# Performance work log

Measured on AMD Instinct MI355X. Metric: run time of the kernel, lower is better.

The kernel has to match this reference:

```python
import jax, jax.numpy as jnp
import numpy as np

L, H, N = 131072, 256, 128
P = N // 2  # conj-symmetric half state


def _hippo_params(p_sz, h_sz):
    # create_DPLR_HiPPO(block_size) in numpy (float64 eigh, then cast)
    n = np.arange(p_sz)
    pv = np.sqrt(1.0 + 2.0 * n)
    A = -(np.tril(np.outer(pv, pv)) - np.diag(n))          # make_HiPPO
    Pl = np.sqrt(n + 0.5)
    Bl = np.sqrt(2.0 * n + 1.0)
    S = A + np.outer(Pl, Pl)                                # normal part
    lam_re = np.full(p_sz, S.diagonal().mean())
    lam_im, V = np.linalg.eigh(S * (-1j))
    Lambda = lam_re + 1j * lam_im                           # (P,)
    Vinv = V.conj().T
    rng = np.random.default_rng(0)
    B0 = rng.normal(size=(p_sz, h_sz)) / np.sqrt(h_sz)      # lecun-normal-ish
    Bc = Vinv @ B0                                          # init_VinvB -> (P,H) complex
    C0 = rng.normal(size=(h_sz, p_sz)) / np.sqrt(p_sz)
    Cc = C0 @ V                                             # init_CV -> (H,P) complex
    Dv = rng.normal(size=(h_sz,))
    return Lambda, Bc, Cc, Dv


def setup_inputs() -> dict:
    Lambda, Bc, Cc, Dv = _hippo_params(P, H)
    deltas = np.logspace(-3.0, -1.0, P)
    key = jax.random.key(0)
    ku, kd = jax.random.split(key)
    u = jax.random.normal(ku, (L, H), dtype=jnp.float32)
    d = jax.random.bernoulli(kd, 1.0 / 1024.0, (L,))        # sparse episode resets
    f32 = lambda a: jnp.asarray(a, dtype=jnp.float32)
    return {
        "u": u,
        "Lambda_re": f32(Lambda.real), "Lambda_im": f32(Lambda.imag),
        "B_re": f32(Bc.real), "B_im": f32(Bc.imag),
        "C_re": f32(Cc.real), "C_im": f32(Cc.imag),
        "D": f32(Dv),
        "deltas": f32(deltas),
        "x0_re": jnp.zeros((P,), jnp.float32), "x0_im": jnp.zeros((P,), jnp.float32),
        "d": d,
    }


def reference(u, Lambda_re, Lambda_im, B_re, B_im, C_re, C_im, D, deltas,
              x0_re, x0_im, d):
    cplx = jnp.complex64
    Lambda = (Lambda_re + 1j * Lambda_im).astype(cplx)      # (P,)
    B = (B_re + 1j * B_im).astype(cplx)                     # (P,H)
    C = (C_re + 1j * C_im).astype(cplx)                     # (H,P)
    x0 = (x0_re + 1j * x0_im).astype(cplx)                  # (P,)

    # ZOH discretization
    Lambda_bar = jnp.exp(Lambda * deltas)                   # (P,)
    B_bar = ((Lambda_bar - 1.0) / Lambda)[:, None] * B      # (P,H)

    Bu = u.astype(cplx) @ B_bar.T                           # (L,P)

    Lseq = u.shape[0]
    A_el = jnp.concatenate([jnp.ones((1, Lambda_bar.shape[0]), cplx),
                            jnp.broadcast_to(Lambda_bar, (Lseq, Lambda_bar.shape[0]))])
    b_el = jnp.concatenate([x0[None, :], Bu])
    d_el = jnp.concatenate([jnp.zeros((1,), bool), d])

    def comb(qi, qj):
        Ai, bi, di = qi
        Aj, bj, dj = qj
        m = dj[..., None]
        A = jnp.where(m, Aj, Aj * Ai)
        b = jnp.where(m, bj, Aj * bi + bj)
        return (A, b, jnp.logical_or(di, dj))

    _, xs, _ = jax.lax.associative_scan(comb, (A_el, b_el, d_el))
    xs = xs[1:]                                             # (L,P)

    # conj-symmetric readout: y = 2*Re(C x) + D*u
    y = 2.0 * (xs @ C.T).real + u * D                       # (L,H)
    return y
```

## Files before the change

### kernel.cpp

```cpp
#include <hip/hip_runtime.h>
#include <hip/hip_bf16.h>
#include <stdint.h>

#define L_SEQ 131072
#define H_DIM 256
#define P_DIM 64
#define C2    128
#define T_CH  128
#define NC    1024
#define SUBT  32
#define BPAD  136

typedef unsigned short u16t;
typedef __attribute__((ext_vector_type(8))) short short8;
typedef __attribute__((ext_vector_type(4))) float f32x4;

#define OFF_W2_U   32768u
#define OFF_LPRE_F 32768u
#define OFF_LPIM_F 40960u
#define OFF_LAMB_F 49152u
#define OFF_FR_I   49408u
#define OFF_CL_F   50432u
#define OFF_XIN_F  181504u
#define OFF_U16_B  2097152u

__device__ __forceinline__ float bf2f(unsigned v){
    return __builtin_bit_cast(float, v << 16);
}
__device__ __forceinline__ u16t f2bf16(float f){
    uint32_t u = __builtin_bit_cast(uint32_t, f);
    u += 0x7fffu + ((u >> 16) & 1u);
    return (u16t)(u >> 16);
}
__device__ __forceinline__ unsigned pk2(float a, float b){
    return (unsigned)f2bf16(a) | ((unsigned)f2bf16(b) << 16);
}

__global__ void k0a(const float* __restrict__ Lre, const float* __restrict__ Lim,
                    const float* __restrict__ deltas, float* __restrict__ wsf){
    int p = threadIdx.x;
    if (p >= P_DIM) return;
    float lr = Lre[p], li = Lim[p], dl = deltas[p];
    float er = expf(lr * dl);
    float si, co;
    sincosf(li * dl, &si, &co);
    float lbr = er * co, lbi = er * si;
    float den = lr*lr + li*li;
    float gr = ((lbr - 1.f)*lr + lbi*li) / den;
    float gi = (lbi*lr - (lbr - 1.f)*li) / den;
    float* lamb = wsf + OFF_LAMB_F;
    lamb[p] = lbr; lamb[64+p] = lbi; lamb[128+p] = gr; lamb[192+p] = gi;
    float* lpre = wsf + OFF_LPRE_F;
    float* lpim = wsf + OFF_LPIM_F;
    float pr = lbr, pi = lbi;
    for (int k = 0; k < T_CH; k++){
        lpre[k*64 + p] = pr;
        lpim[k*64 + p] = pi;
        float nr = pr*lbr - pi*lbi;
        float ni = pr*lbi + pi*lbr;
        pr = nr; pi = ni;
    }
}

__global__ void k0b(const float* __restrict__ Bre, const float* __restrict__ Bim,
                    const float* __restrict__ Cre, const float* __restrict__ Cim,
                    float* __restrict__ wsf, u16t* __restrict__ wsu){
    int idx = blockIdx.x * 256 + threadIdx.x;
    const float* lamb = wsf + OFF_LAMB_F;
    if (idx < 32768){
        int c = idx >> 8, h = idx & 255;
        int p = c & 63;
        float gr = lamb[128+p], gi = lamb[192+p];
        float br = Bre[p*H_DIM + h], bi = Bim[p*H_DIM + h];
        float v = (c < 64) ? (gr*br - gi*bi) : (gr*bi + gi*br);
        wsu[idx] = f2bf16(v);
    } else {
        int i2 = idx - 32768;
        int h = i2 >> 7, c = i2 & 127;
        float v = (c < 64) ? 2.f * Cre[h*P_DIM + c] : -2.f * Cim[h*P_DIM + (c-64)];
        wsu[OFF_W2_U + i2] = f2bf16(v);
    }
}

template<bool WRITE_U16>
__global__ __launch_bounds__(256, 2) void k1(const float* __restrict__ u,
                                             const int* __restrict__ dflag,
                                             float* __restrict__ wsf,
                                             u16t* __restrict__ wsu,
                                             u16t* __restrict__ u16g){
    __shared__ u16t  buf[T_CH * BPAD];
    __shared__ int   d_lds[T_CH];
    __shared__ float sublast[4*128];
    __shared__ int   sfr[4];

    const int tid  = threadIdx.x;
    const int w    = tid >> 6, lane = tid & 63;
    const int m    = lane & 15, q = lane >> 4;
    const int cc   = blockIdx.x;
    const int t0   = cc * T_CH;
    const int tg   = t0 + w * SUBT;

    if (tid < T_CH) d_lds[tid] = dflag[t0 + tid];

    const u16t* W1 = wsu;
    f32x4 acc[2][8];
    #pragma unroll
    for (int a = 0; a < 2; a++)
        #pragma unroll
        for (int b = 0; b < 8; b++) acc[a][b] = (f32x4){0.f,0.f,0.f,0.f};

    #pragma unroll
    for (int kf = 0; kf < 8; kf++){
        const int k0 = kf*32 + q*8;
        short8 afr[2];
        #pragma unroll
        for (int mt = 0; mt < 2; mt++){
            const float* ap = u + (size_t)(tg + mt*16 + m)*H_DIM + k0;
            float4 f0 = *(const float4*)ap;
            float4 f1 = *(const float4*)(ap + 4);
            uint4 pk;
            pk.x = pk2(f0.x, f0.y); pk.y = pk2(f0.z, f0.w);
            pk.z = pk2(f1.x, f1.y); pk.w = pk2(f1.z, f1.w);
            if (WRITE_U16)
                *(uint4*)(u16g + (size_t)(tg + mt*16 + m)*H_DIM + k0) = pk;
            afr[mt] = __builtin_bit_cast(short8, pk);
        }
        #pragma unroll
        for (int nt = 0; nt < 8; nt++){
            short8 bfr = __builtin_bit_cast(short8, *(const uint4*)(W1 + (nt*16 + m)*H_DIM + k0));
            acc[0][nt] = __builtin_amdgcn_mfma_f32_16x16x32_bf16(afr[0], bfr, acc[0][nt], 0,0,0);
            acc[1][nt] = __builtin_amdgcn_mfma_f32_16x16x32_bf16(afr[1], bfr, acc[1][nt], 0,0,0);
        }
    }
    #pragma unroll
    for (int mt = 0; mt < 2; mt++)
        #pragma unroll
        for (int nt = 0; nt < 8; nt++){
            int c  = nt*16 + m;
            int tl = w*SUBT + mt*16 + q*4;
            #pragma unroll
            for (int r = 0; r < 4; r++)
                buf[(tl + r)*BPAD + c] = f2bf16(acc[mt][nt][r]);
        }
    __syncthreads();

    {
        const float* lamb = wsf + OFF_LAMB_F;
        float lbr = lamb[lane], lbi = lamb[64 + lane];
        float xr = 0.f, xi = 0.f;
        int frs = SUBT;
        const int base = w * SUBT;
        for (int tt = 0; tt < SUBT; tt++){
            int tl = base + tt;
            float br = bf2f(buf[tl*BPAD + lane]);
            float bi = bf2f(buf[tl*BPAD + 64 + lane]);
            if (d_lds[tl]){
                if (frs == SUBT) frs = tt;
                xr = br; xi = bi;
            } else {
                float nr = fmaf(lbr, xr, fmaf(-lbi, xi, br));
                float ni = fmaf(lbr, xi, fmaf( lbi, xr, bi));
                xr = nr; xi = ni;
            }
        }
        sublast[w*128 + lane]      = xr;
        sublast[w*128 + 64 + lane] = xi;
        if (lane == 0) sfr[w] = frs;
    }
    __syncthreads();

    if (tid < 64){
        const float* lpre = wsf + OFF_LPRE_F;
        const float* lpim = wsf + OFF_LPIM_F;
        float l32r = lpre[(SUBT-1)*64 + tid], l32i = lpim[(SUBT-1)*64 + tid];
        float xr = 0.f, xi = 0.f;
        int fr_c = T_CH;
        #pragma unroll
        for (int w2 = 0; w2 < 4; w2++){
            float sr = sublast[w2*128 + tid], si = sublast[w2*128 + 64 + tid];
            int f = sfr[w2];
            if (f < SUBT){
                xr = sr; xi = si;
                if (fr_c == T_CH) fr_c = w2*SUBT + f;
            } else {
                float nr = fmaf(l32r, xr, fmaf(-l32i, xi, sr));
                float ni = fmaf(l32r, xi, fmaf( l32i, xr, si));
                xr = nr; xi = ni;
            }
        }
        float* clast = wsf + OFF_CL_F;
        clast[cc*128 + tid]      = xr;
        clast[cc*128 + 64 + tid] = xi;
        if (tid == 0) ((int*)wsf)[OFF_FR_I + cc] = fr_c;
    }
}

__global__ void k2(const float* __restrict__ x0re, const float* __restrict__ x0im,
                   float* __restrict__ wsf){
    const int p = threadIdx.x;
    const float* clast = wsf + OFF_CL_F;
    const int*   frg   = (const int*)wsf + OFF_FR_I;
    float*       xin   = wsf + OFF_XIN_F;
    const float ltr = (wsf + OFF_LPRE_F)[127*64 + p];
    const float lti = (wsf + OFF_LPIM_F)[127*64 + p];
    float xr = x0re[p], xi = x0im[p];
    const int G = 16;
    float br[G], bi[G], br2[G], bi2[G]; int fr[G], fr2[G];

    auto ldg = [&](int cb, float* A, float* B, int* F){
        #pragma unroll
        for (int j = 0; j < G; j++){
            A[j] = clast[(cb+j)*128 + p];
            B[j] = clast[(cb+j)*128 + 64 + p];
            F[j] = frg[cb+j];
        }
    };
    ldg(0, br, bi, fr);
    for (int g = 0; g < NC / G; g++){
        int cb = g * G;
        if (g + 1 < NC / G) ldg(cb + G, br2, bi2, fr2);
        #pragma unroll
        for (int j = 0; j < G; j++){
            xin[(cb+j)*128 + p]      = xr;
            xin[(cb+j)*128 + 64 + p] = xi;
            if (fr[j] < T_CH){ xr = br[j]; xi = bi[j]; }
            else {
                float nr = fmaf(ltr, xr, fmaf(-lti, xi, br[j]));
                float ni = fmaf(ltr, xi, fmaf( lti, xr, bi[j]));
                xr = nr; xi = ni;
            }
        }
        #pragma unroll
        for (int j = 0; j < G; j++){ br[j]=br2[j]; bi[j]=bi2[j]; fr[j]=fr2[j]; }
    }
}

template<bool USE_U16>
__global__ __launch_bounds__(256, 2) void k3(const float* __restrict__ u,
                                             const u16t* __restrict__ u16g,
                                             const int* __restrict__ dflag,
                                             const float* __restrict__ D,
                                             float* __restrict__ wsf,
                                             u16t* __restrict__ wsu,
                                             float* __restrict__ y){
    __shared__ u16t  buf[T_CH * BPAD];
    __shared__ int   d_lds[T_CH];
    __shared__ float sublast[4*128];
    __shared__ float xin_s[4*128];
    __shared__ int   sfr[4];

    const int tid  = threadIdx.x;
    const int w    = tid >> 6, lane = tid & 63;
    const int m    = lane & 15, q = lane >> 4;
    const int cc   = blockIdx.x;
    const int t0   = cc * T_CH;
    const int tg   = t0 + w * SUBT;

    if (tid < T_CH) d_lds[tid] = dflag[t0 + tid];

    {
        const u16t* W1 = wsu;
        f32x4 acc[2][8];
        #pragma unroll
        for (int a = 0; a < 2; a++)
            #pragma unroll
            for (int b = 0; b < 8; b++) acc[a][b] = (f32x4){0.f,0.f,0.f,0.f};

        #pragma unroll
        for (int kf = 0; kf < 8; kf++){
            const int k0 = kf*32 + q*8;
            short8 afr[2];
            #pragma unroll
            for (int mt = 0; mt < 2; mt++){
                if (USE_U16){
                    afr[mt] = __builtin_bit_cast(short8,
                        *(const uint4*)(u16g + (size_t)(tg + mt*16 + m)*H_DIM + k0));
                } else {
                    const float* ap = u + (size_t)(tg + mt*16 + m)*H_DIM + k0;
                    float4 f0 = *(const float4*)ap;
                    float4 f1 = *(const float4*)(ap + 4);
                    uint4 pk;
                    pk.x = pk2(f0.x, f0.y); pk.y = pk2(f0.z, f0.w);
                    pk.z = pk2(f1.x, f1.y); pk.w = pk2(f1.z, f1.w);
                    afr[mt] = __builtin_bit_cast(short8, pk);
                }
            }
            #pragma unroll
            for (int nt = 0; nt < 8; nt++){
                short8 bfr = __builtin_bit_cast(short8, *(const uint4*)(W1 + (nt*16 + m)*H_DIM + k0));
                acc[0][nt] = __builtin_amdgcn_mfma_f32_16x16x32_bf16(afr[0], bfr, acc[0][nt], 0,0,0);
                acc[1][nt] = __builtin_amdgcn_mfma_f32_16x16x32_bf16(afr[1], bfr, acc[1][nt], 0,0,0);
            }
        }
        #pragma unroll
        for (int mt = 0; mt < 2; mt++)
            #pragma unroll
            for (int nt = 0; nt < 8; nt++){
                int c  = nt*16 + m;
                int tl = w*SUBT + mt*16 + q*4;
                #pragma unroll
                for (int r = 0; r < 4; r++)
                    buf[(tl + r)*BPAD + c] = f2bf16(acc[mt][nt][r]);
            }
    }
    __syncthreads();

    {
        const float* lamb = wsf + OFF_LAMB_F;
        float lbr = lamb[lane], lbi = lamb[64 + lane];
        float xr = 0.f, xi = 0.f;
        int frs = SUBT;
        const int base = w * SUBT;
        for (int tt = 0; tt < SUBT; tt++){
            int tl = base + tt;
            float br = bf2f(buf[tl*BPAD + lane]);
            float bi = bf2f(buf[tl*BPAD + 64 + lane]);
            if (d_lds[tl]){
                if (frs == SUBT) frs = tt;
                xr = br; xi = bi;
            } else {
                float nr = fmaf(lbr, xr, fmaf(-lbi, xi, br));
                float ni = fmaf(lbr, xi, fmaf( lbi, xr, bi));
                xr = nr; xi = ni;
            }
            buf[tl*BPAD + lane]      = f2bf16(xr);
            buf[tl*BPAD + 64 + lane] = f2bf16(xi);
        }
        sublast[w*128 + lane]      = xr;
        sublast[w*128 + 64 + lane] = xi;
        if (lane == 0) sfr[w] = frs;
    }
    __syncthreads();

    if (tid < 64){
        const float* lpre = wsf + OFF_LPRE_F;
        const float* lpim = wsf + OFF_LPIM_F;
        const float* xin  = wsf + OFF_XIN_F;
        float l32r = lpre[(SUBT-1)*64 + tid], l32i = lpim[(SUBT-1)*64 + tid];
        float xr = xin[cc*128 + tid], xi = xin[cc*128 + 64 + tid];
        #pragma unroll
        for (int w2 = 0; w2 < 4; w2++){
            xin_s[w2*128 + tid]      = xr;
            xin_s[w2*128 + 64 + tid] = xi;
            float sr = sublast[w2*128 + tid], si = sublast[w2*128 + 64 + tid];
            if (sfr[w2] < SUBT){ xr = sr; xi = si; }
            else {
                float nr = fmaf(l32r, xr, fmaf(-l32i, xi, sr));
                float ni = fmaf(l32r, xi, fmaf( l32i, xr, si));
                xr = nr; xi = ni;
            }
        }
    }
    __syncthreads();

    {
        const float* lpre = wsf + OFF_LPRE_F;
        const float* lpim = wsf + OFF_LPIM_F;
        #pragma unroll 4
        for (int i = 0; i < 32; i++){
            int idx = i*256 + tid;
            int tl = idx >> 6, j = idx & 63;
            int c0 = j*2;
            int w2 = tl >> 5, tt = tl & 31;
            if (tt < sfr[w2]){
                unsigned pr = *(unsigned*)&buf[tl*BPAD + c0];
                float v0 = bf2f(pr & 0xffffu), v1 = bf2f(pr >> 16);
                int p0 = c0 & 63;
                float lr0 = lpre[tt*64 + p0], lr1 = lpre[tt*64 + p0 + 1];
                float li0 = lpim[tt*64 + p0], li1 = lpim[tt*64 + p0 + 1];
                float xr0 = xin_s[w2*128 + p0],      xr1 = xin_s[w2*128 + p0 + 1];
                float xi0 = xin_s[w2*128 + 64 + p0], xi1 = xin_s[w2*128 + 64 + p0 + 1];
                if (c0 < 64){
                    v0 += lr0*xr0 - li0*xi0;
                    v1 += lr1*xr1 - li1*xi1;
                } else {
                    v0 += lr0*xi0 + li0*xr0;
                    v1 += lr1*xi1 + li1*xr1;
                }
                *(unsigned*)&buf[tl*BPAD + c0] = pk2(v0, v1);
            }
        }
    }
    __syncthreads();

    f32x4 acc2[2][16];
    #pragma unroll
    for (int a = 0; a < 2; a++)
        #pragma unroll
        for (int b = 0; b < 16; b++) acc2[a][b] = (f32x4){0.f,0.f,0.f,0.f};
    {
        const u16t* W2 = wsu + OFF_W2_U;
        #pragma unroll
        for (int ng = 0; ng < 4; ng++){
            #pragma unroll
            for (int kf = 0; kf < 4; kf++){
                const int k0 = kf*32 + q*8;
                short8 a0 = *(const short8*)&buf[(w*SUBT +  0 + m)*BPAD + k0];
                short8 a1 = *(const short8*)&buf[(w*SUBT + 16 + m)*BPAD + k0];
                #pragma unroll
                for (int nj = 0; nj < 4; nj++){
                    int nt = ng*4 + nj;
                    short8 bfr = __builtin_bit_cast(short8, *(const uint4*)(W2 + (nt*16 + m)*C2 + k0));
                    acc2[0][nt] = __builtin_amdgcn_mfma_f32_16x16x32_bf16(a0, bfr, acc2[0][nt], 0,0,0);
                    acc2[1][nt] = __builtin_amdgcn_mfma_f32_16x16x32_bf16(a1, bfr, acc2[1][nt], 0,0,0);
                }
            }
        }
    }

    #pragma unroll
    for (int nt = 0; nt < 16; nt++){
        int h = nt*16 + m;
        float dv = D[h];
        #pragma unroll
        for (int mt = 0; mt < 2; mt++){
            int tb = tg + mt*16 + q*4;
            #pragma unroll
            for (int r = 0; r < 4; r++){
                float uv = USE_U16 ? bf2f(u16g[(size_t)(tb + r)*H_DIM + h])
                                   : u[(size_t)(tb + r)*H_DIM + h];
                y[(size_t)(tb + r)*H_DIM + h] = fmaf(uv, dv, acc2[mt][nt][r]);
            }
        }
    }
}

extern "C" void kernel_launch(void* const* d_in, const int* in_sizes, int n_in,
                              void* d_out, int out_size, void* d_ws, size_t ws_size,
                              hipStream_t stream){
    const float* u      = (const float*)d_in[0];
    const float* Lre    = (const float*)d_in[1];
    const float* Lim    = (const float*)d_in[2];
    const float* Bre    = (const float*)d_in[3];
    const float* Bim    = (const float*)d_in[4];
    const float* Cre    = (const float*)d_in[5];
    const float* Cim    = (const float*)d_in[6];
    const float* D      = (const float*)d_in[7];
    const float* x0re   = (const float*)d_in[9];
    const float* x0im   = (const float*)d_in[10];
    const int*   dflag  = (const int*)d_in[11];
    const float* deltas = (const float*)d_in[8];
    float* wsf = (float*)d_ws;
    u16t*  wsu = (u16t*)d_ws;
    u16t*  u16g = (u16t*)((char*)d_ws + OFF_U16_B);
    float* y   = (float*)d_out;

    const size_t need = (size_t)OFF_U16_B + (size_t)L_SEQ * H_DIM * 2;
    const bool use16 = (ws_size >= need);

    k0a<<<1, 64, 0, stream>>>(Lre, Lim, deltas, wsf);
    k0b<<<256, 256, 0, stream>>>(Bre, Bim, Cre, Cim, wsf, wsu);
    if (use16){
        k1<true ><<<NC, 256, 0, stream>>>(u, dflag, wsf, wsu, u16g);
        k2<<<1, 64, 0, stream>>>(x0re, x0im, wsf);
        k3<true ><<<NC, 256, 0, stream>>>(u, u16g, dflag, D, wsf, wsu, y);
    } else {
        k1<false><<<NC, 256, 0, stream>>>(u, dflag, wsf, wsu, u16g);
        k2<<<1, 64, 0, stream>>>(x0re, x0im, wsf);
        k3<false><<<NC, 256, 0, stream>>>(u, u16g, dflag, D, wsf, wsu, y);
    }
}
```

Baseline: 463.1 us.

## Split bf16 conversion into standalone kernel and prefetch all A fragments

The fp32-to-bf16 conversion of u moves out of k1 into a separate grid-stride kernel. k1 then reads the bf16 copy, the same way k3 already did. Both k1 and k3 now load all 16 A-operand fragments into registers before the MFMA loop, so global loads are issued up front rather than interleaved with the matrix math. k1's launch bounds are raised to three blocks per SM. The cost is an extra kernel launch, an extra full pass over u, and higher register pressure from the prefetched fragments.

```diff
diff --git a/kernel.cpp b/kernel.cpp
--- a/kernel.cpp
+++ b/kernel.cpp
@@ -34,6 +34,22 @@
 }
 __device__ __forceinline__ unsigned pk2(float a, float b){
     return (unsigned)f2bf16(a) | ((unsigned)f2bf16(b) << 16);
+}
+
+__global__ __launch_bounds__(256) void kconv(const float* __restrict__ u,
+                                             u16t* __restrict__ o){
+    const size_t n = (size_t)L_SEQ * H_DIM / 8;
+    size_t i = (size_t)blockIdx.x * 256 + threadIdx.x;
+    const size_t step = (size_t)gridDim.x * 256;
+    for (; i < n; i += step){
+        const float* p = u + i*8;
+        float4 a = *(const float4*)p;
+        float4 b = *(const float4*)(p + 4);
+        uint4 o4;
+        o4.x = pk2(a.x, a.y); o4.y = pk2(a.z, a.w);
+        o4.z = pk2(b.x, b.y); o4.w = pk2(b.z, b.w);
+        *(uint4*)(o + i*8) = o4;
+    }
 }
 
 __global__ void k0a(const float* __restrict__ Lre, const float* __restrict__ Lim,
@@ -82,12 +98,12 @@
     }
 }
 
-template<bool WRITE_U16>
-__global__ __launch_bounds__(256, 2) void k1(const float* __restrict__ u,
+template<bool USE_U16>
+__global__ __launch_bounds__(256, 3) void k1(const float* __restrict__ u,
+                                             const u16t* __restrict__ u16g,
                                              const int* __restrict__ dflag,
                                              float* __restrict__ wsf,
-                                             u16t* __restrict__ wsu,
-                                             u16t* __restrict__ u16g){
+                                             u16t* __restrict__ wsu){
     __shared__ u16t  buf[T_CH * BPAD];
     __shared__ int   d_lds[T_CH];
     __shared__ float sublast[4*128];
@@ -102,6 +118,25 @@
 
     if (tid < T_CH) d_lds[tid] = dflag[t0 + tid];
 
+    uint4 ap[16];
+    #pragma unroll
+    for (int kf = 0; kf < 8; kf++){
+        #pragma unroll
+        for (int mt = 0; mt < 2; mt++){
+            if (USE_U16){
+                ap[kf*2+mt] = *(const uint4*)(u16g + (size_t)(tg + mt*16 + m)*H_DIM + kf*32 + q*8);
+            } else {
+                const float* apn = u + (size_t)(tg + mt*16 + m)*H_DIM + kf*32 + q*8;
+                float4 f0 = *(const float4*)apn;
+                float4 f1 = *(const float4*)(apn + 4);
+                uint4 pk;
+                pk.x = pk2(f0.x, f0.y); pk.y = pk2(f0.z, f0.w);
+                pk.z = pk2(f1.x, f1.y); pk.w = pk2(f1.z, f1.w);
+                ap[kf*2+mt] = pk;
+            }
+        }
+    }
+
     const u16t* W1 = wsu;
     f32x4 acc[2][8];
     #pragma unroll
@@ -112,24 +147,13 @@
     #pragma unroll
     for (int kf = 0; kf < 8; kf++){
         const int k0 = kf*32 + q*8;
-        short8 afr[2];
-        #pragma unroll
-        for (int mt = 0; mt < 2; mt++){
-            const float* ap = u + (size_t)(tg + mt*16 + m)*H_DIM + k0;
-            float4 f0 = *(const float4*)ap;
-            float4 f1 = *(const float4*)(ap + 4);
-            uint4 pk;
-            pk.x = pk2(f0.x, f0.y); pk.y = pk2(f0.z, f0.w);
-            pk.z = pk2(f1.x, f1.y); pk.w = pk2(f1.z, f1.w);
-            if (WRITE_U16)
-                *(uint4*)(u16g + (size_t)(tg + mt*16 + m)*H_DIM + k0) = pk;
-            afr[mt] = __builtin_bit_cast(short8, pk);
-        }
+        short8 a0 = __builtin_bit_cast(short8, ap[kf*2+0]);
+        short8 a1 = __builtin_bit_cast(short8, ap[kf*2+1]);
         #pragma unroll
         for (int nt = 0; nt < 8; nt++){
             short8 bfr = __builtin_bit_cast(short8, *(const uint4*)(W1 + (nt*16 + m)*H_DIM + k0));
-            acc[0][nt] = __builtin_amdgcn_mfma_f32_16x16x32_bf16(afr[0], bfr, acc[0][nt], 0,0,0);
-            acc[1][nt] = __builtin_amdgcn_mfma_f32_16x16x32_bf16(afr[1], bfr, acc[1][nt], 0,0,0);
+            acc[0][nt] = __builtin_amdgcn_mfma_f32_16x16x32_bf16(a0, bfr, acc[0][nt], 0,0,0);
+            acc[1][nt] = __builtin_amdgcn_mfma_f32_16x16x32_bf16(a1, bfr, acc[1][nt], 0,0,0);
         }
     }
     #pragma unroll
@@ -259,37 +283,41 @@
     if (tid < T_CH) d_lds[tid] = dflag[t0 + tid];
 
     {
-        const u16t* W1 = wsu;
-        f32x4 acc[2][8];
-        #pragma unroll
-        for (int a = 0; a < 2; a++)
-            #pragma unroll
-            for (int b = 0; b < 8; b++) acc[a][b] = (f32x4){0.f,0.f,0.f,0.f};
-
+        uint4 ap[16];
         #pragma unroll
         for (int kf = 0; kf < 8; kf++){
-            const int k0 = kf*32 + q*8;
-            short8 afr[2];
             #pragma unroll
             for (int mt = 0; mt < 2; mt++){
                 if (USE_U16){
-                    afr[mt] = __builtin_bit_cast(short8,
-                        *(const uint4*)(u16g + (size_t)(tg + mt*16 + m)*H_DIM + k0));
+                    ap[kf*2+mt] = *(const uint4*)(u16g + (size_t)(tg + mt*16 + m)*H_DIM + kf*32 + q*8);
                 } else {
-                    const float* ap = u + (size_t)(tg + mt*16 + m)*H_DIM + k0;
-                    float4 f0 = *(const float4*)ap;
-                    float4 f1 = *(const float4*)(ap + 4);
+                    const float* apn = u + (size_t)(tg + mt*16 + m)*H_DIM + kf*32 + q*8;
+                    float4 f0 = *(const float4*)apn;
+                    float4 f1 = *(const float4*)(apn + 4);
                     uint4 pk;
                     pk.x = pk2(f0.x, f0.y); pk.y = pk2(f0.z, f0.w);
                     pk.z = pk2(f1.x, f1.y); pk.w = pk2(f1.z, f1.w);
-                    afr[mt] = __builtin_bit_cast(short8, pk);
+                    ap[kf*2+mt] = pk;
                 }
             }
+        }
+        const u16t* W1 = wsu;
+        f32x4 acc[2][8];
+        #pragma unroll
+        for (int a = 0; a < 2; a++)
+            #pragma unroll
+            for (int b = 0; b < 8; b++) acc[a][b] = (f32x4){0.f,0.f,0.f,0.f};
+
+        #pragma unroll
+        for (int kf = 0; kf < 8; kf++){
+            const int k0 = kf*32 + q*8;
+            short8 a0 = __builtin_bit_cast(short8, ap[kf*2+0]);
+            short8 a1 = __builtin_bit_cast(short8, ap[kf*2+1]);
             #pragma unroll
             for (int nt = 0; nt < 8; nt++){
                 short8 bfr = __builtin_bit_cast(short8, *(const uint4*)(W1 + (nt*16 + m)*H_DIM + k0));
-                acc[0][nt] = __builtin_amdgcn_mfma_f32_16x16x32_bf16(afr[0], bfr, acc[0][nt], 0,0,0);
-                acc[1][nt] = __builtin_amdgcn_mfma_f32_16x16x32_bf16(afr[1], bfr, acc[1][nt], 0,0,0);
+                acc[0][nt] = __builtin_amdgcn_mfma_f32_16x16x32_bf16(a0, bfr, acc[0][nt], 0,0,0);
+                acc[1][nt] = __builtin_amdgcn_mfma_f32_16x16x32_bf16(a1, bfr, acc[1][nt], 0,0,0);
             }
         }
         #pragma unroll
@@ -451,11 +479,12 @@
     k0a<<<1, 64, 0, stream>>>(Lre, Lim, deltas, wsf);
     k0b<<<256, 256, 0, stream>>>(Bre, Bim, Cre, Cim, wsf, wsu);
     if (use16){
-        k1<true ><<<NC, 256, 0, stream>>>(u, dflag, wsf, wsu, u16g);
+        kconv<<<4096, 256, 0, stream>>>(u, u16g);
+        k1<true ><<<NC, 256, 0, stream>>>(u, u16g, dflag, wsf, wsu);
         k2<<<1, 64, 0, stream>>>(x0re, x0im, wsf);
         k3<true ><<<NC, 256, 0, stream>>>(u, u16g, dflag, D, wsf, wsu, y);
     } else {
-        k1<false><<<NC, 256, 0, stream>>>(u, dflag, wsf, wsu, u16g);
+        k1<false><<<NC, 256, 0, stream>>>(u, u16g, dflag, wsf, wsu);
         k2<<<1, 64, 0, stream>>>(x0re, x0im, wsf);
         k3<false><<<NC, 256, 0, stream>>>(u, u16g, dflag, D, wsf, wsu, y);
     }
```

New measurement: 456.2 us. No clear change (-1.5%).
